# Kernel optimization log

Hardware: AMD Instinct MI355X
Metric: run time of the kernel (lower is better)

Reference implementation:

```python
import jax, jax.numpy as jnp
import numpy as np

OUT = 2048          # rows of sparse weight (out_features)
IN = 2048           # cols of sparse weight (in_features)
NNZ_PER_ROW = 128   # uniform nnz per row -> simple valid CSR indptr
NNZ = OUT * NNZ_PER_ROW
N = 512             # number of input rows (tokens)


def setup_inputs() -> dict:
    key = jax.random.key(0)
    k1, k2, k3 = jax.random.split(key, 3)
    x = jax.random.normal(k1, (N, IN), dtype=jnp.float32)
    data = jax.random.normal(k2, (NNZ,), dtype=jnp.float32)
    # sorted column indices per row (canonical-ish CSR; duplicates are harmless, they sum)
    indices = jnp.sort(
        jax.random.randint(k3, (OUT, NNZ_PER_ROW), 0, IN), axis=1
    ).reshape(NNZ).astype(jnp.int32)
    indptr = (jnp.arange(OUT + 1) * NNZ_PER_ROW).astype(jnp.int32)
    return {"x": x, "data": data, "indices": indices, "indptr": indptr}


def reference(x, data, indices, indptr):
    # CuPyLinear.forward: result = (W_csr @ x.T).T, i.e. y = x @ W.T with W sparse CSR.
    nnz = data.shape[0]
    n_rows = indptr.shape[0] - 1  # static
    # expand CSR indptr to per-nnz row ids
    rows = jnp.searchsorted(indptr, jnp.arange(nnz, dtype=indptr.dtype), side="right") - 1
    # contrib[k, n] = data[k] * x[n, col[k]]
    contrib = data[:, None] * x.T[indices]                 # [nnz, N]
    y_t = jax.ops.segment_sum(contrib, rows, num_segments=n_rows)  # [out, N]
    return y_t.T                                           # [N, out]
```

## Files before the change

kernel.cpp:

```cpp
#include <hip/hip_runtime.h>

#define N_TOK 512
#define IN_F  2048
#define OUT_F 2048
#define NNZ_ROW 128

#define TTOK 4
#define NTILE (N_TOK / TTOK)

#define ROWS 64
#define TPB  32
#define TILES_PB (TPB / TTOK)
#define WPITCH 132
#define YPITCH 36

#define SX_BYTES (IN_F * TTOK * 2)
#define SW_OFF   (2 * SX_BYTES)
#define SW_BYTES (ROWS * WPITCH * 4)
#define SY_OFF   (SW_OFF + SW_BYTES)
#define SY_BYTES (ROWS * YPITCH * 4)
#define SMEM_BYTES (SY_OFF + SY_BYTES)

__device__ ushort g_xt[NTILE * IN_F * TTOK];

static __device__ __forceinline__ unsigned f2bf(float f) {
    unsigned u = __float_as_uint(f);
    return (u + 0x7fffu + ((u >> 16) & 1u)) >> 16;
}

__global__ __launch_bounds__(256) void tile_x(const float* __restrict__ x) {
    const int tile = blockIdx.y;
    const int c    = blockIdx.x * 256 + threadIdx.x;
    const unsigned lo = f2bf(x[(tile * TTOK + 0) * IN_F + c]) |
                        (f2bf(x[(tile * TTOK + 1) * IN_F + c]) << 16);
    const unsigned hi = f2bf(x[(tile * TTOK + 2) * IN_F + c]) |
                        (f2bf(x[(tile * TTOK + 3) * IN_F + c]) << 16);
    ((uint2*)g_xt)[tile * IN_F + c] = make_uint2(lo, hi);
}

__global__ __launch_bounds__(256, 2) void spmm(const float* __restrict__ data,
                                               const int*   __restrict__ indices,
                                               const int*   __restrict__ indptr,
                                               float*       __restrict__ y) {
    extern __shared__ char smem[];
    ushort*   s_x0 = (ushort*)smem;
    ushort*   s_x1 = (ushort*)(smem + SX_BYTES);
    unsigned* s_w  = (unsigned*)(smem + SW_OFF);
    float*    s_y  = (float*)(smem + SY_OFF);

    const int rg = blockIdx.x;
    const int tb = blockIdx.y;
    const int r0 = rg * ROWS;
    const int t  = threadIdx.x;

    const int base0 = indptr[r0];
    const int4*   I4 = (const int4*)(indices + base0);
    const float4* D4 = (const float4*)(data + base0);
#pragma unroll
    for (int i = 0; i < (ROWS * NNZ_ROW / 4) / 256; ++i) {
        const int    e  = t + i * 256;
        const int4   ci = I4[e];
        const float4 dv = D4[e];
        const int    r  = e >> 5;
        const int    m  = e & 31;
        unsigned* dst = s_w + r * WPITCH + m;
        dst[0]  = (__float_as_uint(dv.x) & 0xFFFFF800u) | (unsigned)ci.x;
        dst[33] = (__float_as_uint(dv.y) & 0xFFFFF800u) | (unsigned)ci.y;
        dst[66] = (__float_as_uint(dv.z) & 0xFFFFF800u) | (unsigned)ci.z;
        dst[99] = (__float_as_uint(dv.w) & 0xFFFFF800u) | (unsigned)ci.w;
    }

    auto STAGE_X = [&](ushort* buf, int tile) {
        const char* src = (const char*)g_xt + (size_t)tile * SX_BYTES;
#pragma unroll
        for (int i = 0; i < (SX_BYTES / 16) / 256; ++i) {
            const int off = (t + i * 256) * 16;
            __builtin_amdgcn_global_load_lds((const unsigned*)(src + off),
                                             (unsigned*)((char*)buf + off),
                                             16, 0, 0);
        }
    };

    const int l  = t & 63;
    const int w  = t >> 6;
    const int rw = w * 16 + (l >> 2);
    const int kh = l & 3;
    const unsigned* wrow = s_w + rw * WPITCH + kh * 33;

    STAGE_X(s_x0, tb * TILES_PB);
    __syncthreads();

    for (int ti = 0; ti < TILES_PB; ++ti) {
        ushort* cur = (ti & 1) ? s_x1 : s_x0;
        ushort* nxt = (ti & 1) ? s_x0 : s_x1;
        if (ti + 1 < TILES_PB) STAGE_X(nxt, tb * TILES_PB + ti + 1);

        const uint2* sx = (const uint2*)cur;
        float4 acc = make_float4(0.f, 0.f, 0.f, 0.f);
#pragma unroll 8
        for (int j = 0; j < NNZ_ROW / 4; ++j) {
            const unsigned u  = wrow[j];
            const float    wt = __uint_as_float(u & 0xFFFFF800u);
            const uint2    xv = sx[u & 2047u];
            acc.x += wt * __uint_as_float(xv.x << 16);
            acc.y += wt * __uint_as_float(xv.x);
            acc.z += wt * __uint_as_float(xv.y << 16);
            acc.w += wt * __uint_as_float(xv.y);
        }
        acc.x += __shfl_xor(acc.x, 1); acc.y += __shfl_xor(acc.y, 1);
        acc.z += __shfl_xor(acc.z, 1); acc.w += __shfl_xor(acc.w, 1);
        acc.x += __shfl_xor(acc.x, 2); acc.y += __shfl_xor(acc.y, 2);
        acc.z += __shfl_xor(acc.z, 2); acc.w += __shfl_xor(acc.w, 2);
        if (kh == 0)
            *(float4*)&s_y[rw * YPITCH + ti * TTOK] = acc;
        __syncthreads();
    }

    const int n  = t >> 3;
    const int rb = t & 7;
    float v[8];
#pragma unroll
    for (int j = 0; j < 8; ++j) v[j] = s_y[(rb * 8 + j) * YPITCH + n];
    float* yp = &y[(size_t)(tb * TPB + n) * OUT_F + r0 + rb * 8];
    *(float4*)yp       = make_float4(v[0], v[1], v[2], v[3]);
    *((float4*)yp + 1) = make_float4(v[4], v[5], v[6], v[7]);
}

extern "C" void kernel_launch(void* const* d_in, const int* in_sizes, int n_in,
                              void* d_out, int out_size, void* d_ws, size_t ws_size,
                              hipStream_t stream) {
    const float* x       = (const float*)d_in[0];
    const float* data    = (const float*)d_in[1];
    const int*   indices = (const int*)  d_in[2];
    const int*   indptr  = (const int*)  d_in[3];
    float*       y       = (float*)d_out;

    tile_x<<<dim3(IN_F / 256, NTILE), 256, 0, stream>>>(x);
    spmm<<<dim3(OUT_F / ROWS, N_TOK / TPB), 256, SMEM_BYTES, stream>>>(
        data, indices, indptr, y);
}
```

Baseline: 81.01 us.

## Hold sparse weights in registers per thread instead of packed LDS table

Each thread now loads its own 16 nonzeros (column indices and fp32 weights) into registers and reuses them across all token tiles. This replaces the packed weight/index table in LDS and removes one LDS read per nonzero. Rows per block drop from 64 to 32, with 8 threads per row and an extra shuffle stage for the reduction. The grid doubles, so the x tiles are staged twice as often overall, and the extra registers may lower occupancy. Weights are no longer truncated by the bit-packing, which improves precision.

```diff
diff --git a/kernel.cpp b/kernel.cpp
--- a/kernel.cpp
+++ b/kernel.cpp
@@ -8,18 +8,13 @@
 #define TTOK 4
 #define NTILE (N_TOK / TTOK)
 
-#define ROWS 64
+#define ROWS 32
 #define TPB  32
 #define TILES_PB (TPB / TTOK)
-#define WPITCH 132
+#define KSEG 16
 #define YPITCH 36
 
 #define SX_BYTES (IN_F * TTOK * 2)
-#define SW_OFF   (2 * SX_BYTES)
-#define SW_BYTES (ROWS * WPITCH * 4)
-#define SY_OFF   (SW_OFF + SW_BYTES)
-#define SY_BYTES (ROWS * YPITCH * 4)
-#define SMEM_BYTES (SY_OFF + SY_BYTES)
 
 __device__ ushort g_xt[NTILE * IN_F * TTOK];
 
@@ -38,70 +33,59 @@
     ((uint2*)g_xt)[tile * IN_F + c] = make_uint2(lo, hi);
 }
 
-__global__ __launch_bounds__(256, 2) void spmm(const float* __restrict__ data,
-                                               const int*   __restrict__ indices,
-                                               const int*   __restrict__ indptr,
-                                               float*       __restrict__ y) {
-    extern __shared__ char smem[];
-    ushort*   s_x0 = (ushort*)smem;
-    ushort*   s_x1 = (ushort*)(smem + SX_BYTES);
-    unsigned* s_w  = (unsigned*)(smem + SW_OFF);
-    float*    s_y  = (float*)(smem + SY_OFF);
+__global__ __launch_bounds__(256) void spmm(const float* __restrict__ data,
+                                            const int*   __restrict__ indices,
+                                            const int*   __restrict__ indptr,
+                                            float*       __restrict__ y) {
+    __shared__ ushort s_x[2][IN_F * TTOK];
+    __shared__ float  s_y[ROWS][YPITCH];
 
     const int rg = blockIdx.x;
     const int tb = blockIdx.y;
     const int r0 = rg * ROWS;
     const int t  = threadIdx.x;
+    const int row = t >> 3;
+    const int seg = t & 7;
 
-    const int base0 = indptr[r0];
-    const int4*   I4 = (const int4*)(indices + base0);
-    const float4* D4 = (const float4*)(data + base0);
+    const int base = indptr[r0] + row * NNZ_ROW + seg * KSEG;
+    const int4*   ip = (const int4*)(indices + base);
+    const float4* dp = (const float4*)(data + base);
+    int   cols[KSEG];
+    float wts[KSEG];
 #pragma unroll
-    for (int i = 0; i < (ROWS * NNZ_ROW / 4) / 256; ++i) {
-        const int    e  = t + i * 256;
-        const int4   ci = I4[e];
-        const float4 dv = D4[e];
-        const int    r  = e >> 5;
-        const int    m  = e & 31;
-        unsigned* dst = s_w + r * WPITCH + m;
-        dst[0]  = (__float_as_uint(dv.x) & 0xFFFFF800u) | (unsigned)ci.x;
-        dst[33] = (__float_as_uint(dv.y) & 0xFFFFF800u) | (unsigned)ci.y;
-        dst[66] = (__float_as_uint(dv.z) & 0xFFFFF800u) | (unsigned)ci.z;
-        dst[99] = (__float_as_uint(dv.w) & 0xFFFFF800u) | (unsigned)ci.w;
+    for (int u = 0; u < KSEG / 4; ++u) {
+        const int4   ci = ip[u];
+        const float4 dv = dp[u];
+        cols[4 * u + 0] = ci.x; wts[4 * u + 0] = dv.x;
+        cols[4 * u + 1] = ci.y; wts[4 * u + 1] = dv.y;
+        cols[4 * u + 2] = ci.z; wts[4 * u + 2] = dv.z;
+        cols[4 * u + 3] = ci.w; wts[4 * u + 3] = dv.w;
     }
 
-    auto STAGE_X = [&](ushort* buf, int tile) {
+    auto STAGE_X = [&](int buf, int tile) {
         const char* src = (const char*)g_xt + (size_t)tile * SX_BYTES;
 #pragma unroll
         for (int i = 0; i < (SX_BYTES / 16) / 256; ++i) {
             const int off = (t + i * 256) * 16;
             __builtin_amdgcn_global_load_lds((const unsigned*)(src + off),
-                                             (unsigned*)((char*)buf + off),
+                                             (unsigned*)((char*)s_x[buf] + off),
                                              16, 0, 0);
         }
     };
 
-    const int l  = t & 63;
-    const int w  = t >> 6;
-    const int rw = w * 16 + (l >> 2);
-    const int kh = l & 3;
-    const unsigned* wrow = s_w + rw * WPITCH + kh * 33;
-
-    STAGE_X(s_x0, tb * TILES_PB);
+    STAGE_X(0, tb * TILES_PB);
     __syncthreads();
 
     for (int ti = 0; ti < TILES_PB; ++ti) {
-        ushort* cur = (ti & 1) ? s_x1 : s_x0;
-        ushort* nxt = (ti & 1) ? s_x0 : s_x1;
-        if (ti + 1 < TILES_PB) STAGE_X(nxt, tb * TILES_PB + ti + 1);
+        const int cur = ti & 1;
+        if (ti + 1 < TILES_PB) STAGE_X(cur ^ 1, tb * TILES_PB + ti + 1);
 
-        const uint2* sx = (const uint2*)cur;
+        const uint2* sx = (const uint2*)s_x[cur];
         float4 acc = make_float4(0.f, 0.f, 0.f, 0.f);
-#pragma unroll 8
-        for (int j = 0; j < NNZ_ROW / 4; ++j) {
-            const unsigned u  = wrow[j];
-            const float    wt = __uint_as_float(u & 0xFFFFF800u);
-            const uint2    xv = sx[u & 2047u];
+#pragma unroll
+        for (int j = 0; j < KSEG; ++j) {
+            const uint2 xv = sx[cols[j]];
+            const float wt = wts[j];
             acc.x += wt * __uint_as_float(xv.x << 16);
             acc.y += wt * __uint_as_float(xv.x);
             acc.z += wt * __uint_as_float(xv.y << 16);
@@ -111,19 +95,20 @@
         acc.z += __shfl_xor(acc.z, 1); acc.w += __shfl_xor(acc.w, 1);
         acc.x += __shfl_xor(acc.x, 2); acc.y += __shfl_xor(acc.y, 2);
         acc.z += __shfl_xor(acc.z, 2); acc.w += __shfl_xor(acc.w, 2);
-        if (kh == 0)
-            *(float4*)&s_y[rw * YPITCH + ti * TTOK] = acc;
+        acc.x += __shfl_xor(acc.x, 4); acc.y += __shfl_xor(acc.y, 4);
+        acc.z += __shfl_xor(acc.z, 4); acc.w += __shfl_xor(acc.w, 4);
+        if (seg == 0)
+            *(float4*)&s_y[row][ti * TTOK] = acc;
         __syncthreads();
     }
 
     const int n  = t >> 3;
     const int rb = t & 7;
-    float v[8];
+    float v[4];
 #pragma unroll
-    for (int j = 0; j < 8; ++j) v[j] = s_y[(rb * 8 + j) * YPITCH + n];
-    float* yp = &y[(size_t)(tb * TPB + n) * OUT_F + r0 + rb * 8];
-    *(float4*)yp       = make_float4(v[0], v[1], v[2], v[3]);
-    *((float4*)yp + 1) = make_float4(v[4], v[5], v[6], v[7]);
+    for (int j = 0; j < 4; ++j) v[j] = s_y[rb * 4 + j][n];
+    *(float4*)&y[(size_t)(tb * TPB + n) * OUT_F + r0 + rb * 4] =
+        make_float4(v[0], v[1], v[2], v[3]);
 }
 
 extern "C" void kernel_launch(void* const* d_in, const int* in_sizes, int n_in,
@@ -136,6 +121,6 @@
     float*       y       = (float*)d_out;
 
     tile_x<<<dim3(IN_F / 256, NTILE), 256, 0, stream>>>(x);
-    spmm<<<dim3(OUT_F / ROWS, N_TOK / TPB), 256, SMEM_BYTES, stream>>>(
+    spmm<<<dim3(OUT_F / ROWS, N_TOK / TPB), 256, 0, stream>>>(
         data, indices, indptr, y);
 }
```

After: 81.36 us. No clear change (+0.4%).
